# Kernel optimization log

Measured on AMD Instinct MI355X. Metric: run time of the kernel, lower is better.

Reference implementation:

```python
import jax, jax.numpy as jnp
import numpy as np

H = 16          # n_heads
DH = 128        # head_dim
DR = 64         # rope_dim
DC = DH - DR    # content_dim = 64
THETA = 10000.0
SCALE = 1.0 / np.sqrt(DH)


def _rope_tables(T, dtype):
    inv = 1.0 / (THETA ** (jnp.arange(0, DR, 2, dtype=jnp.float32) / DR))  # [DR/2]
    t = jnp.arange(T, dtype=jnp.float32)
    freqs = jnp.outer(t, inv)  # [T, DR/2]
    return jnp.cos(freqs).astype(dtype), jnp.sin(freqs).astype(dtype)


def _apply_rope(x, cos, sin):
    # x: [B,H,T,DR]; cos/sin: [T,DR/2] broadcast over B,H
    d = x.shape[-1] // 2
    x1, x2 = x[..., :d], x[..., d:]
    return jnp.concatenate([x1 * cos - x2 * sin, x1 * sin + x2 * cos], axis=-1)


def setup_inputs() -> dict:
    key = jax.random.key(0)
    ks = jax.random.split(key, 9)
    B, T, D = 1, 2048, 2048
    s = 0.02
    return {
        "x": jax.random.normal(ks[0], (B, T, D), jnp.float32),
        "Wq_down": jax.random.normal(ks[1], (D, 512), jnp.float32) * s,
        "Wq_up": jax.random.normal(ks[2], (512, H * DC), jnp.float32) * s,
        "Wq_rope": jax.random.normal(ks[3], (D, H * DR), jnp.float32) * s,
        "Wkv_down": jax.random.normal(ks[4], (D, 512), jnp.float32) * s,
        "Wk_up": jax.random.normal(ks[5], (512, H * DC), jnp.float32) * s,
        "Wv_up": jax.random.normal(ks[6], (512, H * DH), jnp.float32) * s,
        "Wk_rope": jax.random.normal(ks[7], (D, H * DR), jnp.float32) * s,
        "Wo": jax.random.normal(ks[8], (H * DH, D), jnp.float32) * s,
    }


def reference(x, Wq_down, Wq_up, Wq_rope, Wkv_down, Wk_up, Wv_up, Wk_rope, Wo):
    B, T, D = x.shape
    # low-rank query path: down then up, content part only
    q_content = ((x @ Wq_down) @ Wq_up).reshape(B, T, H, DC).transpose(0, 2, 1, 3)
    q_pos = (x @ Wq_rope).reshape(B, T, H, DR).transpose(0, 2, 1, 3)
    kv_latent = x @ Wkv_down                    # [B,T,d_latent]
    k_pos = (x @ Wk_rope).reshape(B, T, H, DR).transpose(0, 2, 1, 3)

    cos, sin = _rope_tables(T, x.dtype)
    q_pos = _apply_rope(q_pos, cos, sin)
    k_pos = _apply_rope(k_pos, cos, sin)

    k_content = (kv_latent @ Wk_up).reshape(B, T, H, DC).transpose(0, 2, 1, 3)
    v = (kv_latent @ Wv_up).reshape(B, T, H, DH).transpose(0, 2, 1, 3)

    q = jnp.concatenate([q_content, q_pos], axis=-1)  # [B,H,T,DH]
    k = jnp.concatenate([k_content, k_pos], axis=-1)  # [B,H,T,DH]

    scores = jnp.einsum("bhtd,bhsd->bhts", q, k) * SCALE
    causal = jnp.tril(jnp.ones((T, T), dtype=bool))
    scores = jnp.where(causal, scores, jnp.finfo(scores.dtype).min)
    attn = jax.nn.softmax(scores, axis=-1)
    out = jnp.einsum("bhts,bhsd->bhtd", attn, v)       # [B,H,T,DH]
    out = out.transpose(0, 2, 1, 3).reshape(B, T, H * DH)
    return out @ Wo
```

## Files before the change

### kernel.cpp

```cpp
#include <hip/hip_runtime.h>
#include <math.h>

#define T_SEQ 2048
#define D_MODEL 2048
#define H_HEADS 16
#define DH 128
#define DR 64
#define DC 64
#define D_LAT 512
#define SEGLEN 7
#define NSEG_TOT 46
#define NSEG_OF(q) ((2 * (q) + 2 + SEGLEN - 1) / SEGLEN)
#define QSCALE (0.08838834764831845f * 1.4426950408889634f)

typedef __attribute__((ext_vector_type(8))) short short8;
typedef __attribute__((ext_vector_type(4))) short short4v;
typedef __attribute__((ext_vector_type(4))) float f32x4;

#if __has_builtin(__builtin_amdgcn_exp2f)
#define EXP2(x) __builtin_amdgcn_exp2f(x)
#else
#define EXP2(x) exp2f(x)
#endif

__device__ __forceinline__ float bf2f(short b) {
    unsigned u = ((unsigned)(unsigned short)b) << 16;
    return __builtin_bit_cast(float, u);
}
__device__ __forceinline__ short f2bf(float f) {
    unsigned u = __builtin_bit_cast(unsigned, f);
    unsigned r = u + 0x7fffu + ((u >> 16) & 1u);
    return (short)(r >> 16);
}
__device__ __forceinline__ unsigned f2bf_tru(float f) {
    return __builtin_bit_cast(unsigned, f) >> 16;
}

#define GLD_LDS(gp, lp) \
    __builtin_amdgcn_global_load_lds( \
        (const __attribute__((address_space(1))) void*)(gp), \
        (__attribute__((address_space(3))) void*)(lp), 16, 0, 0)

__device__ __forceinline__ void ct_tile(float (*tile)[33],
                                        const float* __restrict__ W,
                                        short* __restrict__ Wt,
                                        int R, int C, int ldo, int rel) {
    int bx = rel % (C / 32), by = rel / (C / 32);
    int c0 = bx * 32, r0 = by * 32;
    int tx = threadIdx.x & 31, ty = threadIdx.x >> 5;
    #pragma unroll
    for (int i = 0; i < 4; ++i)
        tile[ty + i * 8][tx] = W[(size_t)(r0 + ty + i * 8) * C + c0 + tx];
    __syncthreads();
    #pragma unroll
    for (int i = 0; i < 4; ++i)
        Wt[(size_t)(c0 + ty + i * 8) * ldo + r0 + tx] = f2bf(tile[tx][ty + i * 8]);
    __syncthreads();
}

__global__ __launch_bounds__(256) void prep(const float* __restrict__ x,
                                            short* __restrict__ xb,
                                            const float* __restrict__ Wqd,
                                            const float* __restrict__ Wkvd,
                                            const float* __restrict__ Wqr,
                                            const float* __restrict__ Wkr,
                                            const float* __restrict__ Wqu,
                                            const float* __restrict__ Wku,
                                            const float* __restrict__ Wvu,
                                            const float* __restrict__ Wo,
                                            short* __restrict__ WdT,
                                            short* __restrict__ WupT2,
                                            short* __restrict__ WoT) {
    __shared__ float tile[32][33];
    int bid = blockIdx.x;
    if (bid < 4096) {
        int i = bid * 1024 + threadIdx.x * 4;
        float4 f = *(const float4*)&x[i];
        short4v o;
        o.x = f2bf(f.x); o.y = f2bf(f.y); o.z = f2bf(f.z); o.w = f2bf(f.w);
        *(short4v*)&xb[i] = o;
    } else if (bid < 5120) {
        ct_tile(tile, Wqd,  WdT + (size_t)0 * 2048,    2048, 512,  2048, bid - 4096);
    } else if (bid < 6144) {
        ct_tile(tile, Wkvd, WdT + (size_t)512 * 2048,  2048, 512,  2048, bid - 5120);
    } else if (bid < 8192) {
        ct_tile(tile, Wqr,  WdT + (size_t)1024 * 2048, 2048, 1024, 2048, bid - 6144);
    } else if (bid < 10240) {
        ct_tile(tile, Wkr,  WdT + (size_t)2048 * 2048, 2048, 1024, 2048, bid - 8192);
    } else if (bid < 10752) {
        ct_tile(tile, Wqu,  WupT2 + (size_t)0 * 512,    512, 1024, 512, bid - 10240);
    } else if (bid < 11264) {
        ct_tile(tile, Wku,  WupT2 + (size_t)1024 * 512, 512, 1024, 512, bid - 10752);
    } else if (bid < 12288) {
        ct_tile(tile, Wvu,  WupT2 + (size_t)2048 * 512, 512, 2048, 512, bid - 11264);
    } else {
        ct_tile(tile, Wo,   WoT, 2048, 2048, 2048, bid - 12288);
    }
}

__global__ __launch_bounds__(256) void transpose_bf16(const short* __restrict__ in,
                                                      short* __restrict__ vTc,
                                                      int ldi) {
    __shared__ short tile[64][65];
    int c0 = blockIdx.x * 64, t0 = blockIdx.y * 64;
    int tx = threadIdx.x & 31, ty = threadIdx.x >> 5;
    #pragma unroll
    for (int i = 0; i < 8; ++i) {
        int r = ty + i * 8;
        int vv = *(const int*)&in[(size_t)(t0 + r) * ldi + c0 + tx * 2];
        tile[r][tx * 2]     = (short)(vv & 0xffff);
        tile[r][tx * 2 + 1] = (short)(((unsigned)vv) >> 16);
    }
    __syncthreads();
    #pragma unroll
    for (int i = 0; i < 8; ++i) {
        int G = i * 256 + threadIdx.x;
        int ch2 = G >> 10;
        int rem = G & 1023;
        int dl = rem >> 4;
        int mp = rem & 15;
        int dval = c0 + dl;
        int h = dval >> 7, d128 = dval & 127;
        int g  = (mp >> 2) ^ (d128 & 3);
        int mi = mp & 3;
        int kl = 4 * g + 2 * (mi & 1) + 16 * (mi >> 1);
        unsigned lo = (unsigned short)tile[ch2 * 32 + kl][dl];
        unsigned hi = (unsigned short)tile[ch2 * 32 + kl + 1][dl];
        int chg = (t0 >> 5) + ch2;
        size_t off = ((size_t)(h * 64 + chg)) * 4096 + d128 * 32 + mp * 2;
        *(int*)&vTc[off] = (int)(lo | (hi << 16));
    }
}

__global__ __launch_bounds__(256) void gemm_bt(const short* __restrict__ A,
                                               const short* __restrict__ A2,
                                               const short* __restrict__ Bt,
                                               short* __restrict__ C0,
                                               short* __restrict__ C1,
                                               short* __restrict__ C2,
                                               short* __restrict__ C3,
                                               int N, int Kblk,
                                               int lda, int ldb, int ldc,
                                               int ncut, int scut, float cscale) {
    __shared__ short As[128 * 64];
    __shared__ short Bs[128 * 64];
    const int tid = threadIdx.x;
    const int wave = tid >> 6, lane = tid & 63;
    const int lin = blockIdx.x;
    const int X = N >> 7, Xq = X >> 2;
    const int xcd = lin & 7;
    int r = lin >> 3;
    const int bx = (xcd & 3) * Xq + (r % Xq); r /= Xq;
    const int by = (xcd >> 2) * 8 + (r & 7);
    const int bz = r >> 3;
    const int row0 = by * 128, col0 = bx * 128;
    const int kbase = bz * Kblk;
    const short* Ause = (col0 < ncut) ? A : A2;
    short* Cuse = (bz == 0) ? C0 : (bz == 1) ? C1 : (bz == 2) ? C2 : C3;
    const int wr = (wave >> 1) * 64, wc = (wave & 1) * 64;
    const int lr = lane & 15, quad = lane >> 4;

    f32x4 acc[4][4];
    #pragma unroll
    for (int i = 0; i < 4; ++i)
        #pragma unroll
        for (int j = 0; j < 4; ++j) acc[i][j] = (f32x4){0.f, 0.f, 0.f, 0.f};

    for (int k0 = kbase; k0 < kbase + Kblk; k0 += 64) {
        __syncthreads();
        #pragma unroll
        for (int it = 0; it < 4; ++it) {
            int idx = wave * 64 + it * 256 + lane;
            int row = idx >> 3;
            int scg = (idx & 7) ^ (row & 7);
            const short* ga = Ause + (size_t)(row0 + row) * lda + k0 + scg * 8;
            const short* gb = Bt   + (size_t)(col0 + row) * ldb + k0 + scg * 8;
            int lds0 = (wave * 64 + it * 256) * 8;
            GLD_LDS(ga, &As[lds0]);
            GLD_LDS(gb, &Bs[lds0]);
        }
        __syncthreads();

        #pragma unroll
        for (int kk = 0; kk < 2; ++kk) {
            short8 af[4], bfr[4];
            #pragma unroll
            for (int i = 0; i < 4; ++i)
                af[i] = *(const short8*)
                    &As[(wr + i * 16 + lr) * 64 + (((kk * 4 + quad) ^ (lr & 7)) * 8)];
            #pragma unroll
            for (int j = 0; j < 4; ++j)
                bfr[j] = *(const short8*)
                    &Bs[(wc + j * 16 + lr) * 64 + (((kk * 4 + quad) ^ (lr & 7)) * 8)];
            #pragma unroll
            for (int i = 0; i < 4; ++i)
                #pragma unroll
                for (int j = 0; j < 4; ++j)
                    acc[i][j] = __builtin_amdgcn_mfma_f32_16x16x32_bf16(
                        af[i], bfr[j], acc[i][j], 0, 0, 0);
        }
    }

    const float sc = (col0 < scut) ? cscale : 1.0f;
    #pragma unroll
    for (int i = 0; i < 4; ++i) {
        int rb = row0 + wr + i * 16 + quad * 4;
        #pragma unroll
        for (int j = 0; j < 4; ++j) {
            int c = col0 + wc + j * 16 + lr;
            #pragma unroll
            for (int rr = 0; rr < 4; ++rr)
                Cuse[(size_t)(rb + rr) * ldc + c] = f2bf(acc[i][j][rr] * sc);
        }
    }
}

__device__ __forceinline__ void stage_tile256(const short* __restrict__ Ause,
                                              const short* __restrict__ Bt,
                                              int row0, int col0, int k0,
                                              int lda, int ldb,
                                              short* As, short* Bs, int tid) {
    #pragma unroll
    for (int it = 0; it < 4; ++it) {
        int idx = it * 512 + tid;
        int row = idx >> 3;
        int scg = (idx & 7) ^ (row & 7);
        GLD_LDS(Ause + (size_t)(row0 + row) * lda + k0 + scg * 8, &As[idx * 8]);
    }
    #pragma unroll
    for (int it = 0; it < 2; ++it) {
        int idx = it * 512 + tid;
        int row = idx >> 3;
        int scg = (idx & 7) ^ (row & 7);
        GLD_LDS(Bt + (size_t)(col0 + row) * ldb + k0 + scg * 8, &Bs[idx * 8]);
    }
}

__global__ __launch_bounds__(512) void gemm256_bt(const short* __restrict__ A,
                                                  const short* __restrict__ A2,
                                                  const short* __restrict__ Bt,
                                                  short* __restrict__ C0,
                                                  short* __restrict__ C1,
                                                  int nbx, int Kblk,
                                                  int lda, int ldb, int ldc,
                                                  int ncut, int scut, float cscale) {
    __shared__ short As3[3][256 * 64];
    __shared__ short Bs3[3][128 * 64];
    const int tid = threadIdx.x;
    const int wave = tid >> 6, lane = tid & 63;
    const int lr = lane & 15, quad = lane >> 4;
    const int wm = wave >> 1, wn = wave & 1;

    const int lin = blockIdx.x;
    const int by = lin & 7;
    const int rem = lin >> 3;
    const int bx = rem % nbx;
    const int bz = rem / nbx;
    const int row0 = by * 256, col0 = bx * 128;
    const int kbase = bz * Kblk;
    const short* Ause = (col0 < ncut) ? A : A2;
    short* Cuse = (bz == 0) ? C0 : C1;
    const int NT = Kblk >> 6;

    f32x4 acc[4][4];
    #pragma unroll
    for (int i = 0; i < 4; ++i)
        #pragma unroll
        for (int j = 0; j < 4; ++j) acc[i][j] = (f32x4){0.f, 0.f, 0.f, 0.f};

    #pragma unroll
    for (int tt = 0; tt < 3; ++tt)
        stage_tile256(Ause, Bt, row0, col0, kbase + tt * 64, lda, ldb,
                      &As3[tt][0], &Bs3[tt][0], tid);

    int b = 0;
    for (int t = 0; t < NT; ++t) {
        const int ahead = NT - 1 - t;
        if (ahead >= 2)      asm volatile("s_waitcnt vmcnt(12)" ::: "memory");
        else if (ahead == 1) asm volatile("s_waitcnt vmcnt(6)"  ::: "memory");
        else                 asm volatile("s_waitcnt vmcnt(0)"  ::: "memory");
        __builtin_amdgcn_s_barrier();
        asm volatile("" ::: "memory");

        const short* Ab = &As3[b][0];
        const short* Bb = &Bs3[b][0];
        short8 af[4][2], bfv[4][2];
        #pragma unroll
        for (int fi = 0; fi < 4; ++fi) {
            int rowa = wm * 64 + fi * 16 + lr;
            #pragma unroll
            for (int kk = 0; kk < 2; ++kk)
                af[fi][kk] = *(const short8*)
                    &Ab[rowa * 64 + (((kk * 4 + quad) ^ (lr & 7)) * 8)];
        }
        #pragma unroll
        for (int fj = 0; fj < 4; ++fj) {
            int rowb = wn * 64 + fj * 16 + lr;
            #pragma unroll
            for (int kk = 0; kk < 2; ++kk)
                bfv[fj][kk] = *(const short8*)
                    &Bb[rowb * 64 + (((kk * 4 + quad) ^ (lr & 7)) * 8)];
        }
        #pragma unroll
        for (int fi = 0; fi < 4; ++fi)
            #pragma unroll
            for (int fj = 0; fj < 4; ++fj)
                #pragma unroll
                for (int kk = 0; kk < 2; ++kk)
                    acc[fi][fj] = __builtin_amdgcn_mfma_f32_16x16x32_bf16(
                        af[fi][kk], bfv[fj][kk], acc[fi][fj], 0, 0, 0);

        asm volatile("" ::: "memory");
        __builtin_amdgcn_s_barrier();
        asm volatile("" ::: "memory");
        if (t + 3 < NT)
            stage_tile256(Ause, Bt, row0, col0, kbase + (t + 3) * 64, lda, ldb,
                          &As3[b][0], &Bs3[b][0], tid);
        b = (b == 2) ? 0 : b + 1;
    }

    const float sc = (col0 < scut) ? cscale : 1.0f;
    #pragma unroll
    for (int fi = 0; fi < 4; ++fi) {
        int rb = row0 + wm * 64 + fi * 16 + quad * 4;
        #pragma unroll
        for (int fj = 0; fj < 4; ++fj) {
            int c = col0 + wn * 64 + fj * 16 + lr;
            #pragma unroll
            for (int rr = 0; rr < 4; ++rr)
                Cuse[(size_t)(rb + rr) * ldc + c] = f2bf(acc[fi][fj][rr] * sc);
        }
    }
}

__global__ __launch_bounds__(192) void finish_down(short* __restrict__ cat,
                                                   const short* __restrict__ pdown) {
    const int t = blockIdx.x;
    const int k8 = threadIdx.x * 8;
    const int c0 = ((k8 >> 5) << 6) + (k8 & 31);
    const size_t lo = (size_t)t * 3072 + c0;
    const size_t hi = lo + 32;
    short8 al = *(const short8*)&cat[lo];
    short8 ah = *(const short8*)&cat[hi];
    short8 bl = *(const short8*)&pdown[lo];
    short8 bh = *(const short8*)&pdown[hi];
    float xl[8], xh[8];
    #pragma unroll
    for (int j = 0; j < 8; ++j) {
        xl[j] = bf2f(al[j]) + bf2f(bl[j]);
        xh[j] = bf2f(ah[j]) + bf2f(bh[j]);
    }
    if (c0 >= 1024) {
        float sc = (c0 < 2048) ? QSCALE : 1.0f;
        #pragma unroll
        for (int j = 0; j < 8; ++j) {
            int i = (c0 & 31) + j;
            float freq = (float)t * __powf(10000.0f, -(float)i / 32.0f);
            float cs = __cosf(freq), sn = __sinf(freq);
            float r1 = (xl[j] * cs - xh[j] * sn) * sc;
            float r2 = (xl[j] * sn + xh[j] * cs) * sc;
            xl[j] = r1; xh[j] = r2;
        }
    }
    short8 ol, oh;
    #pragma unroll
    for (int j = 0; j < 8; ++j) { ol[j] = f2bf(xl[j]); oh[j] = f2bf(xh[j]); }
    *(short8*)&cat[lo] = ol;
    *(short8*)&cat[hi] = oh;
}

__global__ __launch_bounds__(256) void add_out_f32(const short* __restrict__ p0,
                                                   const short* __restrict__ p1,
                                                   float* __restrict__ out) {
    int i = (blockIdx.x * 256 + threadIdx.x) * 4;
    short4v a = *(const short4v*)&p0[i];
    short4v b = *(const short4v*)&p1[i];
    float4 o;
    o.x = bf2f(a.x) + bf2f(b.x);
    o.y = bf2f(a.y) + bf2f(b.y);
    o.z = bf2f(a.z) + bf2f(b.z);
    o.w = bf2f(a.w) + bf2f(b.w);
    *(float4*)&out[i] = o;
}

__global__ __launch_bounds__(256) void attn_mla_split(const short* __restrict__ qkup,
                                                      const short* __restrict__ cat,
                                                      const short* __restrict__ vTc,
                                                      short* __restrict__ slabA,
                                                      short* __restrict__ slabB,
                                                      float* __restrict__ lpart) {
    const int lin = blockIdx.x;
    const int xcd = lin & 7;
    int k_ = lin >> 3;
    const int h = xcd + 8 * (k_ & 1);
    const int pp = k_ >> 1;
    int qt = 0, s = 0, acc = 0;
    #pragma unroll
    for (int q = 0; q < 16; ++q) {
        const int ns = NSEG_OF(q);
        if (pp >= acc) { qt = q; s = pp - acc; }
        acc += ns;
    }
    const int nchunk = 2 * qt + 2;
    const int nsq = NSEG_OF(qt);
    const int cbase = nchunk / nsq, crem = nchunk % nsq;
    const int c0 = s * cbase + (s < crem ? s : crem);
    const int c1 = c0 + cbase + (s < crem ? 1 : 0);

    const int tid = threadIdx.x;
    const int wave = tid >> 6, lane = tid & 63;
    const int lr = lane & 15, quad = lane >> 4;

    __shared__ short Ks[2][32 * 128];
    __shared__ short Vst[2][128 * 32];

    const short8 ones = {0x3F80, 0x3F80, 0x3F80, 0x3F80,
                         0x3F80, 0x3F80, 0x3F80, 0x3F80};

    const int Q0 = qt * 128;
    const int qrowA = Q0 + wave * 16;
    const int qrowB = qrowA + 64;

    short8 qf[2][4];
    #pragma unroll
    for (int sb = 0; sb < 2; ++sb) {
        int t = (sb ? qrowB : qrowA) + lr;
        #pragma unroll
        for (int kci = 0; kci < 4; ++kci) {
            const short* src = (kci < 2)
                ? qkup + (size_t)t * 4096 + h * 64
                : cat + (size_t)t * 3072 + 1024 + h * 64;
            qf[sb][kci] = *(const short8*)&src[(kci & 1) * 32 + quad * 8];
        }
    }

    const int idx = wave * 64 + lane;
    const int key = idx >> 4;
    const int cg = (idx & 15) ^ (key & 15);
    const short* kp0 = (cg < 8)
        ? qkup + (size_t)key * 4096 + 1024 + h * 64 + cg * 8
        : cat + (size_t)key * 3072 + 2048 + h * 64 + (cg - 8) * 8;
    const int kst = (cg < 8) ? 4096 : 3072;
    const short* kp1 = kp0 + (size_t)16 * kst;
    const short* vp0 = vTc + ((size_t)h * 64 + (size_t)c0 * 2) * 4096 + idx * 8;
    kp0 += (size_t)c0 * 64 * kst; kp1 += (size_t)c0 * 64 * kst;
    const int kadv = 64 * kst;
    const int kph = 32 * kst;
    const int ldsA = (wave * 64) * 8;
    const int ldsB = (wave * 64 + 256) * 8;

    f32x4 Oacc[2][8];
    #pragma unroll
    for (int sb = 0; sb < 2; ++sb)
        #pragma unroll
        for (int d = 0; d < 8; ++d) Oacc[sb][d] = (f32x4){0.f, 0.f, 0.f, 0.f};
    f32x4 Lacc[2];
    Lacc[0] = (f32x4){0.f, 0.f, 0.f, 0.f};
    Lacc[1] = (f32x4){0.f, 0.f, 0.f, 0.f};

    for (int cc = c0; cc < c1; ++cc) {
        __syncthreads();
        GLD_LDS(kp0,        &Ks[0][ldsA]);
        GLD_LDS(kp1,        &Ks[0][ldsB]);
        GLD_LDS(kp0 + kph,  &Ks[1][ldsA]);
        GLD_LDS(kp1 + kph,  &Ks[1][ldsB]);
        GLD_LDS(vp0,        &Vst[0][ldsA]);
        GLD_LDS(vp0 + 2048, &Vst[0][ldsB]);
        GLD_LDS(vp0 + 4096, &Vst[1][ldsA]);
        GLD_LDS(vp0 + 6144, &Vst[1][ldsB]);
        kp0 += kadv; kp1 += kadv; vp0 += 8192;
        __syncthreads();

        #pragma unroll
        for (int half = 0; half < 2; ++half) {
            const int s0 = cc * 64 + half * 32;
            if (s0 > qrowB + 15) continue;
            const bool actA = (s0 <= qrowA + 15);
            const short* Kc = Ks[half];
            const short* Vc = Vst[half];

            f32x4 sacc[2][2];
            #pragma unroll
            for (int sb = 0; sb < 2; ++sb)
                #pragma unroll
                for (int n = 0; n < 2; ++n) sacc[sb][n] = (f32x4){0.f, 0.f, 0.f, 0.f};
            #pragma unroll
            for (int n = 0; n < 2; ++n) {
                #pragma unroll
                for (int kci = 0; kci < 4; ++kci) {
                    short8 kf = *(const short8*)
                        &Kc[(n * 16 + lr) * 128 + ((kci * 4 + quad) ^ lr) * 8];
                    if (actA)
                        sacc[0][n] = __builtin_amdgcn_mfma_f32_16x16x32_bf16(
                            kf, qf[0][kci], sacc[0][n], 0, 0, 0);
                    sacc[1][n] = __builtin_amdgcn_mfma_f32_16x16x32_bf16(
                        kf, qf[1][kci], sacc[1][n], 0, 0, 0);
                }
            }
            short8 paA, paB;
            #pragma unroll
            for (int sb = 0; sb < 2; ++sb) {
                if (sb == 0 && !actA) continue;
                const int qrow0 = sb ? qrowB : qrowA;
                if (s0 + 31 > qrow0) {
                    #pragma unroll
                    for (int n = 0; n < 2; ++n) {
                        #pragma unroll
                        for (int r = 0; r < 4; ++r) {
                            int kidx = s0 + n * 16 + quad * 4 + r;
                            sacc[sb][n][r] = (kidx <= qrow0 + lr)
                                           ? sacc[sb][n][r] : -1e30f;
                        }
                    }
                }
                int4 pw;
                pw.x = (int)(f2bf_tru(EXP2(sacc[sb][0][0])) |
                             (f2bf_tru(EXP2(sacc[sb][0][1])) << 16));
                pw.y = (int)(f2bf_tru(EXP2(sacc[sb][0][2])) |
                             (f2bf_tru(EXP2(sacc[sb][0][3])) << 16));
                pw.z = (int)(f2bf_tru(EXP2(sacc[sb][1][0])) |
                             (f2bf_tru(EXP2(sacc[sb][1][1])) << 16));
                pw.w = (int)(f2bf_tru(EXP2(sacc[sb][1][2])) |
                             (f2bf_tru(EXP2(sacc[sb][1][3])) << 16));
                if (sb) paB = __builtin_bit_cast(short8, pw);
                else    paA = __builtin_bit_cast(short8, pw);
            }
            if (actA)
                Lacc[0] = __builtin_amdgcn_mfma_f32_16x16x32_bf16(paA, ones,
                                                                  Lacc[0], 0, 0, 0);
            Lacc[1] = __builtin_amdgcn_mfma_f32_16x16x32_bf16(paB, ones,
                                                              Lacc[1], 0, 0, 0);
            #pragma unroll
            for (int dt = 0; dt < 8; ++dt) {
                short8 vf = *(const short8*)
                    &Vc[(dt * 16 + lr) * 32 + (quad ^ (lr & 3)) * 8];
                if (actA)
                    Oacc[0][dt] = __builtin_amdgcn_mfma_f32_16x16x32_bf16(
                        paA, vf, Oacc[0][dt], 0, 0, 0);
                Oacc[1][dt] = __builtin_amdgcn_mfma_f32_16x16x32_bf16(
                    paB, vf, Oacc[1][dt], 0, 0, 0);
            }
        }
    }

    const int slot = h * NSEG_TOT + pp;
    short* slotp = (slot < 512) ? slabA + (size_t)slot * 16384
                                : slabB + (size_t)(slot - 512) * 16384;
    #pragma unroll
    for (int sb = 0; sb < 2; ++sb) {
        const int rbase = wave * 16 + sb * 64 + quad * 4;
        #pragma unroll
        for (int r = 0; r < 4; ++r) {
            #pragma unroll
            for (int dt = 0; dt < 8; ++dt)
                slotp[(rbase + r) * 128 + dt * 16 + lr] = f2bf(Oacc[sb][dt][r]);
        }
        if (lr == 0) {
            #pragma unroll
            for (int r = 0; r < 4; ++r)
                lpart[(size_t)slot * 128 + rbase + r] = Lacc[sb][r];
        }
    }
}

__global__ __launch_bounds__(256) void attn_combine(const short* __restrict__ slabA,
                                                    const short* __restrict__ slabB,
                                                    const float* __restrict__ lpart,
                                                    short* __restrict__ ao) {
    const int t = blockIdx.x;
    const int qt = t >> 7, rl = t & 127;
    const int h = threadIdx.x >> 4;
    const int di = (threadIdx.x & 15) * 8;
    int pf = 0;
    #pragma unroll
    for (int q = 0; q < 16; ++q)
        if (q < qt) pf += NSEG_OF(q);
    const int ns = NSEG_OF(qt);
    float o[8] = {0.f, 0.f, 0.f, 0.f, 0.f, 0.f, 0.f, 0.f};
    float den = 0.f;
    for (int s = 0; s < ns; ++s) {
        const int slot = h * NSEG_TOT + pf + s;
        const short* sp = (slot < 512) ? slabA + (size_t)slot * 16384
                                       : slabB + (size_t)(slot - 512) * 16384;
        short8 v = *(const short8*)&sp[rl * 128 + di];
        #pragma unroll
        for (int j = 0; j < 8; ++j) o[j] += bf2f(v[j]);
        den += lpart[(size_t)slot * 128 + rl];
    }
    float inv = 1.0f / den;
    short8 ov;
    #pragma unroll
    for (int j = 0; j < 8; ++j) ov[j] = f2bf(o[j] * inv);
    *(short8*)&ao[(size_t)t * 2048 + h * 128 + di] = ov;
}

extern "C" void kernel_launch(void* const* d_in, const int* in_sizes, int n_in,
                              void* d_out, int out_size, void* d_ws, size_t ws_size,
                              hipStream_t stream) {
    const float* x        = (const float*)d_in[0];
    const float* Wq_down  = (const float*)d_in[1];
    const float* Wq_up    = (const float*)d_in[2];
    const float* Wq_rope  = (const float*)d_in[3];
    const float* Wkv_down = (const float*)d_in[4];
    const float* Wk_up    = (const float*)d_in[5];
    const float* Wv_up    = (const float*)d_in[6];
    const float* Wk_rope  = (const float*)d_in[7];
    const float* Wo       = (const float*)d_in[8];
    float* out = (float*)d_out;

    short* p = (short*)d_ws;
    short* xb     = p; p += (size_t)2048 * 2048;
    short* WoT    = p; p += (size_t)2048 * 2048;
    short* cat    = p; p += (size_t)2048 * 3072;
    short* upcat2 = p; p += (size_t)2048 * 4096;
    short* WdT    = p; p += (size_t)3072 * 2048;
    short* WupT2  = p; p += (size_t)4096 * 512;
    short* vTc    = p; p += (size_t)2048 * 2048;
    float* lpart  = (float*)p;
    short* pdown   = upcat2;
    short* aob     = cat;
    short* slabA   = WdT;
    short* slabB   = xb;
    short* pw0     = upcat2;
    short* pw1     = upcat2 + (size_t)2048 * 2048;

    prep<<<dim3(16384), 256, 0, stream>>>(x, xb, Wq_down, Wkv_down, Wq_rope,
                                          Wk_rope, Wq_up, Wk_up, Wv_up, Wo,
                                          WdT, WupT2, WoT);

    gemm_bt<<<dim3(24 * 16 * 2), 256, 0, stream>>>(xb, xb, WdT, cat, pdown,
                                                   nullptr, nullptr,
                                                   3072, 1024,
                                                   2048, 2048, 3072, 1 << 30, 0, 1.f);

    finish_down<<<dim3(2048), 192, 0, stream>>>(cat, pdown);

    gemm256_bt<<<dim3(256), 512, 0, stream>>>(cat, cat + 512, WupT2,
                                              upcat2, nullptr,
                                              32, 512,
                                              3072, 512, 4096, 1024, 1024, QSCALE);

    transpose_bf16<<<dim3(32, 32), 256, 0, stream>>>(upcat2 + 2048, vTc, 4096);

    attn_mla_split<<<dim3(16 * NSEG_TOT), 256, 0, stream>>>(upcat2, cat, vTc,
                                                            slabA, slabB, lpart);
    attn_combine<<<dim3(2048), 256, 0, stream>>>(slabA, slabB, lpart, aob);

    gemm256_bt<<<dim3(256), 512, 0, stream>>>(aob, aob, WoT,
                                              pw0, pw1,
                                              16, 1024,
                                              2048, 2048, 2048, 1 << 30, 0, 1.f);
    add_out_f32<<<dim3(2048 * 2048 / 1024), 256, 0, stream>>>(pw0, pw1, out);
}
```

Before: 253.8 us.

## Replace split-K down-projection GEMM with 256-tile GEMM and drop partial-sum pass

The down-projection (x times the concatenated down/rope weights) used to run as a 128x128-tile GEMM split over K into two partial outputs, followed by a kernel that added the partials and applied RoPE. It now runs on the triple-buffered 256-tile GEMM over the full K, with 192 blocks writing one output. The follow-up kernel only applies RoPE and scaling to the rope columns. This removes the write and re-read of a partial buffer and one elementwise add pass. In exchange there are fewer blocks (192 on a GPU with more CUs) and each block does a longer K loop, so some CUs may sit idle.

```diff
diff --git a/kernel.cpp b/kernel.cpp
--- a/kernel.cpp
+++ b/kernel.cpp
@@ -132,89 +132,6 @@
     }
 }
 
-__global__ __launch_bounds__(256) void gemm_bt(const short* __restrict__ A,
-                                               const short* __restrict__ A2,
-                                               const short* __restrict__ Bt,
-                                               short* __restrict__ C0,
-                                               short* __restrict__ C1,
-                                               short* __restrict__ C2,
-                                               short* __restrict__ C3,
-                                               int N, int Kblk,
-                                               int lda, int ldb, int ldc,
-                                               int ncut, int scut, float cscale) {
-    __shared__ short As[128 * 64];
-    __shared__ short Bs[128 * 64];
-    const int tid = threadIdx.x;
-    const int wave = tid >> 6, lane = tid & 63;
-    const int lin = blockIdx.x;
-    const int X = N >> 7, Xq = X >> 2;
-    const int xcd = lin & 7;
-    int r = lin >> 3;
-    const int bx = (xcd & 3) * Xq + (r % Xq); r /= Xq;
-    const int by = (xcd >> 2) * 8 + (r & 7);
-    const int bz = r >> 3;
-    const int row0 = by * 128, col0 = bx * 128;
-    const int kbase = bz * Kblk;
-    const short* Ause = (col0 < ncut) ? A : A2;
-    short* Cuse = (bz == 0) ? C0 : (bz == 1) ? C1 : (bz == 2) ? C2 : C3;
-    const int wr = (wave >> 1) * 64, wc = (wave & 1) * 64;
-    const int lr = lane & 15, quad = lane >> 4;
-
-    f32x4 acc[4][4];
-    #pragma unroll
-    for (int i = 0; i < 4; ++i)
-        #pragma unroll
-        for (int j = 0; j < 4; ++j) acc[i][j] = (f32x4){0.f, 0.f, 0.f, 0.f};
-
-    for (int k0 = kbase; k0 < kbase + Kblk; k0 += 64) {
-        __syncthreads();
-        #pragma unroll
-        for (int it = 0; it < 4; ++it) {
-            int idx = wave * 64 + it * 256 + lane;
-            int row = idx >> 3;
-            int scg = (idx & 7) ^ (row & 7);
-            const short* ga = Ause + (size_t)(row0 + row) * lda + k0 + scg * 8;
-            const short* gb = Bt   + (size_t)(col0 + row) * ldb + k0 + scg * 8;
-            int lds0 = (wave * 64 + it * 256) * 8;
-            GLD_LDS(ga, &As[lds0]);
-            GLD_LDS(gb, &Bs[lds0]);
-        }
-        __syncthreads();
-
-        #pragma unroll
-        for (int kk = 0; kk < 2; ++kk) {
-            short8 af[4], bfr[4];
-            #pragma unroll
-            for (int i = 0; i < 4; ++i)
-                af[i] = *(const short8*)
-                    &As[(wr + i * 16 + lr) * 64 + (((kk * 4 + quad) ^ (lr & 7)) * 8)];
-            #pragma unroll
-            for (int j = 0; j < 4; ++j)
-                bfr[j] = *(const short8*)
-                    &Bs[(wc + j * 16 + lr) * 64 + (((kk * 4 + quad) ^ (lr & 7)) * 8)];
-            #pragma unroll
-            for (int i = 0; i < 4; ++i)
-                #pragma unroll
-                for (int j = 0; j < 4; ++j)
-                    acc[i][j] = __builtin_amdgcn_mfma_f32_16x16x32_bf16(
-                        af[i], bfr[j], acc[i][j], 0, 0, 0);
-        }
-    }
-
-    const float sc = (col0 < scut) ? cscale : 1.0f;
-    #pragma unroll
-    for (int i = 0; i < 4; ++i) {
-        int rb = row0 + wr + i * 16 + quad * 4;
-        #pragma unroll
-        for (int j = 0; j < 4; ++j) {
-            int c = col0 + wc + j * 16 + lr;
-            #pragma unroll
-            for (int rr = 0; rr < 4; ++rr)
-                Cuse[(size_t)(rb + rr) * ldc + c] = f2bf(acc[i][j][rr] * sc);
-        }
-    }
-}
-
 __device__ __forceinline__ void stage_tile256(const short* __restrict__ Ause,
                                               const short* __restrict__ Bt,
                                               int row0, int col0, int k0,
@@ -333,34 +250,29 @@
     }
 }
 
-__global__ __launch_bounds__(192) void finish_down(short* __restrict__ cat,
-                                                   const short* __restrict__ pdown) {
+__global__ __launch_bounds__(128) void rope_qk(short* __restrict__ cat) {
     const int t = blockIdx.x;
     const int k8 = threadIdx.x * 8;
-    const int c0 = ((k8 >> 5) << 6) + (k8 & 31);
+    const int c0 = 1024 + ((k8 >> 5) << 6) + (k8 & 31);
     const size_t lo = (size_t)t * 3072 + c0;
     const size_t hi = lo + 32;
     short8 al = *(const short8*)&cat[lo];
     short8 ah = *(const short8*)&cat[hi];
-    short8 bl = *(const short8*)&pdown[lo];
-    short8 bh = *(const short8*)&pdown[hi];
     float xl[8], xh[8];
     #pragma unroll
     for (int j = 0; j < 8; ++j) {
-        xl[j] = bf2f(al[j]) + bf2f(bl[j]);
-        xh[j] = bf2f(ah[j]) + bf2f(bh[j]);
-    }
-    if (c0 >= 1024) {
-        float sc = (c0 < 2048) ? QSCALE : 1.0f;
-        #pragma unroll
-        for (int j = 0; j < 8; ++j) {
-            int i = (c0 & 31) + j;
-            float freq = (float)t * __powf(10000.0f, -(float)i / 32.0f);
-            float cs = __cosf(freq), sn = __sinf(freq);
-            float r1 = (xl[j] * cs - xh[j] * sn) * sc;
-            float r2 = (xl[j] * sn + xh[j] * cs) * sc;
-            xl[j] = r1; xh[j] = r2;
-        }
+        xl[j] = bf2f(al[j]);
+        xh[j] = bf2f(ah[j]);
+    }
+    float sc = (c0 < 2048) ? QSCALE : 1.0f;
+    #pragma unroll
+    for (int j = 0; j < 8; ++j) {
+        int i = (c0 & 31) + j;
+        float freq = (float)t * __powf(10000.0f, -(float)i / 32.0f);
+        float cs = __cosf(freq), sn = __sinf(freq);
+        float r1 = (xl[j] * cs - xh[j] * sn) * sc;
+        float r2 = (xl[j] * sn + xh[j] * cs) * sc;
+        xl[j] = r1; xh[j] = r2;
     }
     short8 ol, oh;
     #pragma unroll
@@ -617,7 +529,6 @@
     short* WupT2  = p; p += (size_t)4096 * 512;
     short* vTc    = p; p += (size_t)2048 * 2048;
     float* lpart  = (float*)p;
-    short* pdown   = upcat2;
     short* aob     = cat;
     short* slabA   = WdT;
     short* slabB   = xb;
@@ -628,12 +539,11 @@
                                           Wk_rope, Wq_up, Wk_up, Wv_up, Wo,
                                           WdT, WupT2, WoT);
 
-    gemm_bt<<<dim3(24 * 16 * 2), 256, 0, stream>>>(xb, xb, WdT, cat, pdown,
-                                                   nullptr, nullptr,
-                                                   3072, 1024,
-                                                   2048, 2048, 3072, 1 << 30, 0, 1.f);
-
-    finish_down<<<dim3(2048), 192, 0, stream>>>(cat, pdown);
+    gemm256_bt<<<dim3(192), 512, 0, stream>>>(xb, xb, WdT, cat, nullptr,
+                                              24, 2048,
+                                              2048, 2048, 3072, 1 << 30, 0, 1.f);
+
+    rope_qk<<<dim3(2048), 128, 0, stream>>>(cat);
 
     gemm256_bt<<<dim3(256), 512, 0, stream>>>(cat, cat + 512, WupT2,
                                               upcat2, nullptr,
```

New measurement: 264.0 us. 4.0% more time.
